# Optimization experiments

Hardware: AMD Instinct MI355X
Metric: run time of the kernel (lower is better)

The kernel has to match this reference:

```python
import jax, jax.numpy as jnp
import numpy as np

N = 50000
E = 800000
NODE_F = 128
HID = 96
TEMP_F = 10


def setup_inputs() -> dict:
    key = jax.random.key(0)
    ks = jax.random.split(key, 10)
    x = jax.random.normal(ks[0], (N, NODE_F), dtype=jnp.float32)
    edge_index = jax.random.randint(ks[1], (2, E), 0, N, dtype=jnp.int64)
    temporal = jax.random.normal(ks[2], (N, TEMP_F), dtype=jnp.float32)
    # GCNConv: lin weight [in, out] (no bias in lin), separate bias [out]
    W_gcn = jax.random.normal(ks[3], (NODE_F, HID), dtype=jnp.float32) / np.sqrt(NODE_F)
    b_gcn = jnp.zeros((HID,), dtype=jnp.float32)
    W1 = jax.random.normal(ks[4], (HID + TEMP_F, HID), dtype=jnp.float32) / np.sqrt(HID + TEMP_F)
    b1 = jax.random.normal(ks[5], (HID,), dtype=jnp.float32) * 0.01
    W2 = jax.random.normal(ks[6], (HID + NODE_F, 1), dtype=jnp.float32) / np.sqrt(HID + NODE_F)
    b2 = jax.random.normal(ks[7], (1,), dtype=jnp.float32) * 0.01
    return {"x": x, "edge_index": edge_index, "temporal": temporal,
            "W_gcn": W_gcn, "b_gcn": b_gcn, "W1": W1, "b1": b1, "W2": W2, "b2": b2}


def _gcn_conv(x, edge_index, W, b):
    n = x.shape[0]
    loop = jnp.arange(n, dtype=edge_index.dtype)
    src = jnp.concatenate([edge_index[0], loop])  # [E+N]
    dst = jnp.concatenate([edge_index[1], loop])
    # symmetric normalization with self-loops (PyG gcn_norm)
    ones = jnp.ones(src.shape[0], dtype=x.dtype)
    deg = jax.ops.segment_sum(ones, dst, num_segments=n)
    dinv = jnp.where(deg > 0, jax.lax.rsqrt(deg), 0.0)
    norm = dinv[src] * dinv[dst]  # [E+N]
    h = x @ W  # [N, HID]
    msg = h[src] * norm[:, None]  # [E+N, HID] gather + scale
    out = jax.ops.segment_sum(msg, dst, num_segments=n)  # scatter-add
    return out + b


def reference(x, edge_index, temporal, W_gcn, b_gcn, W1, b1, W2, b2):
    h = jax.nn.relu(_gcn_conv(x, edge_index, W_gcn, b_gcn))  # [N, HID]
    h = jnp.concatenate([h, temporal], axis=-1)              # [N, HID+TEMP_F]
    h = jax.nn.relu(h @ W1 + b1)                             # [N, HID]
    h = jnp.concatenate([h, x], axis=-1)                     # [N, HID+NODE_F]
    return jax.nn.relu(h @ W2 + b2)                          # [N, 1]
```

## Files before the change

### kernel.cpp

```cpp
#include <hip/hip_runtime.h>
#include <hip/hip_bf16.h>

#define NN 50000
#define NPAD 50048
#define NE 800000
#define NF 128
#define HH 96
#define TF 10
#define Z1DIM (HH + TF)
#define ZK 128
#define NCH 4
#define CW 24
#define CWP 32
#define NBK 196
#define CAP 5120
#define EPB 2048
#define FILLA_B ((NE + EPB - 1) / EPB)

#define WBLK (NF * HH / 4 / 256)
#define W1BLK (HH * ZK / 4 / 256)
#define ZPAD_JOBS 3
#define GEMM_JOBS (NPAD / 64)
#define AGG_JOBS (8 * 782)

typedef __attribute__((ext_vector_type(8))) short short8;
typedef __attribute__((ext_vector_type(8))) unsigned short ushort8;
typedef __attribute__((ext_vector_type(4))) float f32x4;

__device__ __forceinline__ float bu2f(unsigned short u) {
    union { unsigned int i; float f; } c;
    c.i = ((unsigned int)u) << 16;
    return c.f;
}
__device__ __forceinline__ unsigned short f2bu(float f) {
    union { __hip_bfloat16 h; unsigned short u; } c;
    c.h = __float2bfloat16(f);
    return c.u;
}
__device__ __forceinline__ float u2f32(unsigned short lo, unsigned short hi) {
    union { unsigned int i; float f; } c;
    c.i = ((unsigned int)hi << 16) | lo;
    return c.f;
}

__global__ void k_init(int* __restrict__ bcur, int* __restrict__ off) {
    int t = threadIdx.x;
    if (t < NBK) bcur[t] = t * CAP;
    if (t == 255) off[NN] = NE;
}

__global__ __launch_bounds__(256) void k_pre(const int* __restrict__ ei,
                                             int* __restrict__ bcur,
                                             int* __restrict__ temp,
                                             const float* __restrict__ W,
                                             const float* __restrict__ W1,
                                             unsigned short* __restrict__ Wt,
                                             unsigned short* __restrict__ Wt1,
                                             unsigned short* __restrict__ zb) {
    const int t = threadIdx.x;
    if (blockIdx.x < FILLA_B) {
        __shared__ int hist[NBK], bas[NBK];
        for (int m = t; m < NBK; m += 256) hist[m] = 0;
        __syncthreads();
        const int e0 = blockIdx.x * EPB;
        const int ecap = min(e0 + EPB, NE);
        for (int e = e0 + t; e < ecap; e += 256) {
            int d = ei[NE + e];
            atomicAdd(&hist[d >> 8], 1);
        }
        __syncthreads();
        for (int m = t; m < NBK; m += 256) {
            int c = hist[m];
            bas[m] = c ? atomicAdd(&bcur[m], c) : 0;
            hist[m] = 0;
        }
        __syncthreads();
        for (int e = e0 + t; e < ecap; e += 256) {
            int d = ei[NE + e], s = ei[e];
            int b = d >> 8;
            int r = atomicAdd(&hist[b], 1);
            temp[bas[b] + r] = ((d & 255) << 16) | s;
        }
        return;
    }
    int b = blockIdx.x - FILLA_B;
    if (b < WBLK) {
        int e = (b * 256 + t) * 4;
        int n = e >> 7, k = e & 127;
        ushort4 v;
        v.x = f2bu(W[(k + 0) * HH + n]);
        v.y = f2bu(W[(k + 1) * HH + n]);
        v.z = f2bu(W[(k + 2) * HH + n]);
        v.w = f2bu(W[(k + 3) * HH + n]);
        *(ushort4*)(Wt + e) = v;
    } else if (b < WBLK + W1BLK) {
        int e = ((b - WBLK) * 256 + t) * 4;
        int n = e >> 7, k = e & 127;
        ushort4 v;
        v.x = (k + 0 < Z1DIM) ? f2bu(W1[(k + 0) * HH + n]) : (unsigned short)0;
        v.y = (k + 1 < Z1DIM) ? f2bu(W1[(k + 1) * HH + n]) : (unsigned short)0;
        v.z = (k + 2 < Z1DIM) ? f2bu(W1[(k + 2) * HH + n]) : (unsigned short)0;
        v.w = (k + 3 < Z1DIM) ? f2bu(W1[(k + 3) * HH + n]) : (unsigned short)0;
        *(ushort4*)(Wt1 + e) = v;
    } else {
        int e8 = ((b - WBLK - W1BLK) * 256 + t) * 8;
        ushort8 z = {};
        *(ushort8*)(zb + (size_t)NN * ZK + e8) = z;
    }
}

__global__ __launch_bounds__(256) void k_gg(const int* __restrict__ temp,
                                            const int* __restrict__ bcur,
                                            unsigned short* __restrict__ csr,
                                            int* __restrict__ off,
                                            const float* __restrict__ x,
                                            const unsigned short* __restrict__ Wt,
                                            const float* __restrict__ W2,
                                            unsigned short* __restrict__ hp_c,
                                            float* __restrict__ xw2) {
    const int t = threadIdx.x;
    if (blockIdx.x < NBK) {
        __shared__ int ls[256], lc[256];
        const int b = blockIdx.x;
        int szt = (t < NBK) ? (bcur[t] - t * CAP) : 0;
        ls[t] = szt;
        __syncthreads();
#pragma unroll
        for (int d = 1; d < 256; d <<= 1) {
            int u = (t >= d) ? ls[t - d] : 0;
            __syncthreads();
            ls[t] += u;
            __syncthreads();
        }
        const int g0 = (b > 0) ? ls[b - 1] : 0;
        __syncthreads();
        ls[t] = 0;
        __syncthreads();
        const int seg0 = b * CAP;
        const int m = bcur[b] - seg0;
        for (int k = t; k < m; k += 256) atomicAdd(&ls[temp[seg0 + k] >> 16], 1);
        __syncthreads();
        const int myc = ls[t];
        lc[t] = myc;
        __syncthreads();
#pragma unroll
        for (int d = 1; d < 256; d <<= 1) {
            int u = (t >= d) ? lc[t - d] : 0;
            __syncthreads();
            lc[t] += u;
            __syncthreads();
        }
        const int myoff = g0 + lc[t] - myc;
        __syncthreads();
        lc[t] = myoff;
        const int i = b * 256 + t;
        if (i < NN) {
            off[i] = myoff;
            const float dinv = rsqrtf((float)myc + 1.f);
#pragma unroll
            for (int cc = 0; cc < NCH; ++cc)
                *(float*)(hp_c + (size_t)cc * NN * CWP + (size_t)i * CWP + 28) = dinv;
        } else if (i == NN) {
            off[NN] = NE;
        }
        __syncthreads();
        for (int k = t; k < m; k += 256) {
            int v = temp[seg0 + k];
            int r = atomicAdd(&lc[v >> 16], 1);
            csr[r] = (unsigned short)(v & 0xFFFF);
        }
        return;
    }
    const int wave = t >> 6;
    const int lane = t & 63;
    const int quad = lane >> 4;
    const int l16 = lane & 15;
    const int Mbase = (blockIdx.x - NBK) * 64 + wave * 16;
    const int row = Mbase + l16;
    const bool valid = row < NN;

    const float* xr = x + (size_t)row * NF + quad * 8;
    const unsigned short* brow = Wt + (size_t)l16 * NF + quad * 8;

    f32x4 acc[6] = {};
    float xs = 0.f;
#pragma unroll
    for (int ks = 0; ks < 4; ++ks) {
        short8 a = {};
        if (valid) {
            float4 f0 = *(const float4*)(xr + ks * 32);
            float4 f1 = *(const float4*)(xr + ks * 32 + 4);
            const float4 w0 = *(const float4*)(W2 + HH + quad * 8 + ks * 32);
            const float4 w1 = *(const float4*)(W2 + HH + quad * 8 + ks * 32 + 4);
            xs = fmaf(f0.x, w0.x, xs); xs = fmaf(f0.y, w0.y, xs);
            xs = fmaf(f0.z, w0.z, xs); xs = fmaf(f0.w, w0.w, xs);
            xs = fmaf(f1.x, w1.x, xs); xs = fmaf(f1.y, w1.y, xs);
            xs = fmaf(f1.z, w1.z, xs); xs = fmaf(f1.w, w1.w, xs);
            a[0] = (short)f2bu(f0.x); a[1] = (short)f2bu(f0.y);
            a[2] = (short)f2bu(f0.z); a[3] = (short)f2bu(f0.w);
            a[4] = (short)f2bu(f1.x); a[5] = (short)f2bu(f1.y);
            a[6] = (short)f2bu(f1.z); a[7] = (short)f2bu(f1.w);
        }
#pragma unroll
        for (int nt = 0; nt < 6; ++nt) {
            short8 bfrag = *(const short8*)(brow + (size_t)nt * 16 * NF + ks * 32);
            acc[nt] = __builtin_amdgcn_mfma_f32_16x16x32_bf16(a, bfrag, acc[nt], 0, 0, 0);
        }
    }
    xs += __shfl_xor(xs, 16, 64);
    xs += __shfl_xor(xs, 32, 64);
    if (quad == 0 && valid) xw2[row] = xs;

    const int r0 = Mbase + quad * 4;
#pragma unroll
    for (int nt = 0; nt < 6; ++nt) {
        int n = nt * 16 + l16;
        int c = n / CW, jj = n - c * CW;
        unsigned short* dst = hp_c + (size_t)c * NN * CWP + jj;
#pragma unroll
        for (int k = 0; k < 4; ++k)
            if (r0 + k < NN) dst[(size_t)(r0 + k) * CWP] = f2bu(acc[nt][k]);
    }
}

__global__ __launch_bounds__(256) void k_agg(const unsigned short* __restrict__ hp_c,
                                             const int* __restrict__ off,
                                             const unsigned short* __restrict__ csr,
                                             const float* __restrict__ bg,
                                             const float* __restrict__ tmp,
                                             unsigned short* __restrict__ zb) {
    const int b = blockIdx.x;
    const int slot = b & 7;
    const int c = slot >> 1;
    const int r = (b >> 3) * 2 + (slot & 1);
    const int item = r * 256 + threadIdx.x;
    if (item >= NN * 8) return;
    const int i = item >> 3;
    const int sub = item & 7;
    const int q = sub & 3;
    const int h = sub >> 2;
    const int lane = threadIdx.x & 63;
    const int srcl = lane | 3;
    const unsigned short* __restrict__ base = hp_c + (size_t)c * NN * CWP + q * 8;

    float a[8];
    if (h == 0) {
        ushort8 sv = *(const ushort8*)(base + (size_t)i * CWP);
        float dsl = __shfl(u2f32(sv[4], sv[5]), srcl, 64);
#pragma unroll
        for (int j = 0; j < 8; ++j) a[j] = dsl * bu2f(sv[j]);
    } else {
#pragma unroll
        for (int j = 0; j < 8; ++j) a[j] = 0.f;
    }

    const int start = off[i];
    const int end = off[i + 1];
    const int len = end - start;
    const float dv = rsqrtf((float)len + 1.f);
    const int half0 = (len + 1) >> 1;
    int k = h ? start + half0 : start;
    const int ke = h ? end : start + half0;
    for (; k + 3 < ke; k += 4) {
        int s0 = csr[k], s1 = csr[k + 1], s2 = csr[k + 2], s3 = csr[k + 3];
        ushort8 v0 = *(const ushort8*)(base + (size_t)s0 * CWP);
        ushort8 v1 = *(const ushort8*)(base + (size_t)s1 * CWP);
        ushort8 v2 = *(const ushort8*)(base + (size_t)s2 * CWP);
        ushort8 v3 = *(const ushort8*)(base + (size_t)s3 * CWP);
        float d0 = __shfl(u2f32(v0[4], v0[5]), srcl, 64);
        float d1 = __shfl(u2f32(v1[4], v1[5]), srcl, 64);
        float d2 = __shfl(u2f32(v2[4], v2[5]), srcl, 64);
        float d3 = __shfl(u2f32(v3[4], v3[5]), srcl, 64);
#pragma unroll
        for (int j = 0; j < 8; ++j) {
            float p0 = fmaf(d0, bu2f(v0[j]), a[j]);
            float p1 = fmaf(d2, bu2f(v2[j]), fmaf(d1, bu2f(v1[j]), 0.f));
            a[j] = fmaf(d3, bu2f(v3[j]), p0 + p1);
        }
    }
    for (; k < ke; ++k) {
        ushort8 v0 = *(const ushort8*)(base + (size_t)csr[k] * CWP);
        float d0 = __shfl(u2f32(v0[4], v0[5]), srcl, 64);
#pragma unroll
        for (int j = 0; j < 8; ++j) a[j] = fmaf(d0, bu2f(v0[j]), a[j]);
    }
#pragma unroll
    for (int j = 0; j < 8; ++j) a[j] += __shfl_xor(a[j], 4, 64);
    if (h == 0) {
        if (q < 3) {
            const int j0 = c * CW + q * 8;
            ushort8 o;
#pragma unroll
            for (int j = 0; j < 8; ++j)
                o[j] = f2bu(fmaxf(fmaf(dv, a[j], bg[j0 + j]), 0.f));
            *(ushort8*)(zb + (size_t)i * ZK + j0) = o;
        } else if (c == 3) {
            const float* tp = tmp + (size_t)i * TF;
            ushort8 o0, z = {};
#pragma unroll
            for (int j = 0; j < 8; ++j) o0[j] = f2bu(tp[j]);
            ushort8 o1 = z;
            o1[0] = f2bu(tp[8]);
            o1[1] = f2bu(tp[9]);
            unsigned short* zp = zb + (size_t)i * ZK + HH;
            *(ushort8*)(zp) = o0;
            *(ushort8*)(zp + 8) = o1;
            *(ushort8*)(zp + 16) = z;
            *(ushort8*)(zp + 24) = z;
        }
    }
}

__global__ __launch_bounds__(256) void k_mlp2(const unsigned short* __restrict__ zb,
                                              const unsigned short* __restrict__ Wt1,
                                              const float* __restrict__ b1,
                                              const float* __restrict__ W2,
                                              const float* __restrict__ b2,
                                              const float* __restrict__ xw2,
                                              float* __restrict__ out) {
    const int wave = threadIdx.x >> 6;
    const int lane = threadIdx.x & 63;
    const int quad = lane >> 4;
    const int l16 = lane & 15;
    const int Mbase = blockIdx.x * 64 + wave * 16;

    const unsigned short* arow = zb + (size_t)(Mbase + l16) * ZK + quad * 8;
    const unsigned short* brow = Wt1 + (size_t)l16 * ZK + quad * 8;

    f32x4 acc[6] = {};
#pragma unroll
    for (int ks = 0; ks < 4; ++ks) {
        short8 a = *(const short8*)(arow + ks * 32);
#pragma unroll
        for (int nt = 0; nt < 6; ++nt) {
            short8 bfrag = *(const short8*)(brow + (size_t)nt * 16 * ZK + ks * 32);
            acc[nt] = __builtin_amdgcn_mfma_f32_16x16x32_bf16(a, bfrag, acc[nt], 0, 0, 0);
        }
    }
    float bb[6], wa[6];
#pragma unroll
    for (int nt = 0; nt < 6; ++nt) {
        int c = nt * 16 + l16;
        bb[nt] = b1[c];
        wa[nt] = W2[c];
    }
    const float bias2 = b2[0];

#pragma unroll
    for (int reg = 0; reg < 4; ++reg) {
        const int r = Mbase + quad * 4 + reg;
        float p = 0.f;
#pragma unroll
        for (int nt = 0; nt < 6; ++nt)
            p = fmaf(fmaxf(acc[nt][reg] + bb[nt], 0.f), wa[nt], p);
#pragma unroll
        for (int m = 1; m < 16; m <<= 1) p += __shfl_xor(p, m, 64);
        if (l16 == 0 && r < NN) out[r] = fmaxf(p + xw2[r] + bias2, 0.f);
    }
}

extern "C" void kernel_launch(void* const* d_in, const int* in_sizes, int n_in,
                              void* d_out, int out_size, void* d_ws, size_t ws_size,
                              hipStream_t stream) {
    const float* x   = (const float*)d_in[0];
    const int*   ei  = (const int*)d_in[1];
    const float* tmp = (const float*)d_in[2];
    const float* Wg  = (const float*)d_in[3];
    const float* bg  = (const float*)d_in[4];
    const float* W1  = (const float*)d_in[5];
    const float* b1  = (const float*)d_in[6];
    const float* W2  = (const float*)d_in[7];
    const float* b2  = (const float*)d_in[8];
    float* out = (float*)d_out;

    char* base = (char*)d_ws;
    int* off  = (int*)base;
    int* bcur = (int*)(base + (256 << 10));
    unsigned short* csr = (unsigned short*)(base + (512 << 10));
    unsigned short* Wt  = (unsigned short*)(base + ((size_t)3 << 20));
    unsigned short* Wt1 = Wt + NF * HH;
    unsigned short* hp_c = (unsigned short*)(base + ((size_t)4 << 20));
    unsigned short* zb  = (unsigned short*)(base + ((size_t)17 << 20));
    float* xw2 = (float*)(base + ((size_t)30 << 20));
    int* temp  = (int*)(base + ((size_t)31 << 20));

    k_init <<<1, 256, 0, stream>>>(bcur, off);
    k_pre  <<<FILLA_B + WBLK + W1BLK + ZPAD_JOBS, 256, 0, stream>>>(
                ei, bcur, temp, Wg, W1, Wt, Wt1, zb);
    k_gg   <<<NBK + GEMM_JOBS, 256, 0, stream>>>(temp, bcur, csr, off, x, Wt, W2, hp_c, xw2);
    k_agg  <<<AGG_JOBS, 256, 0, stream>>>(hp_c, off, csr, bg, tmp, zb);
    k_mlp2 <<<GEMM_JOBS, 256, 0, stream>>>(zb, Wt1, b1, W2, b2, xw2, out);
}
```

Before: 169.2 us.

## Fuse GCN aggregation with MLP stage through shared-memory tile

```diff
diff --git a/kernel.cpp b/kernel.cpp
--- a/kernel.cpp
+++ b/kernel.cpp
@@ -19,9 +19,8 @@
 
 #define WBLK (NF * HH / 4 / 256)
 #define W1BLK (HH * ZK / 4 / 256)
-#define ZPAD_JOBS 3
 #define GEMM_JOBS (NPAD / 64)
-#define AGG_JOBS (8 * 782)
+#define ZTS 136
 
 typedef __attribute__((ext_vector_type(8))) short short8;
 typedef __attribute__((ext_vector_type(8))) unsigned short ushort8;
@@ -43,10 +42,9 @@
     return c.f;
 }
 
-__global__ void k_init(int* __restrict__ bcur, int* __restrict__ off) {
+__global__ void k_init(int* __restrict__ bcur) {
     int t = threadIdx.x;
     if (t < NBK) bcur[t] = t * CAP;
-    if (t == 255) off[NN] = NE;
 }
 
 __global__ __launch_bounds__(256) void k_pre(const int* __restrict__ ei,
@@ -55,8 +53,7 @@
                                              const float* __restrict__ W,
                                              const float* __restrict__ W1,
                                              unsigned short* __restrict__ Wt,
-                                             unsigned short* __restrict__ Wt1,
-                                             unsigned short* __restrict__ zb) {
+                                             unsigned short* __restrict__ Wt1) {
     const int t = threadIdx.x;
     if (blockIdx.x < FILLA_B) {
         __shared__ int hist[NBK], bas[NBK];
@@ -93,7 +90,7 @@
         v.z = f2bu(W[(k + 2) * HH + n]);
         v.w = f2bu(W[(k + 3) * HH + n]);
         *(ushort4*)(Wt + e) = v;
-    } else if (b < WBLK + W1BLK) {
+    } else {
         int e = ((b - WBLK) * 256 + t) * 4;
         int n = e >> 7, k = e & 127;
         ushort4 v;
@@ -102,10 +99,6 @@
         v.z = (k + 2 < Z1DIM) ? f2bu(W1[(k + 2) * HH + n]) : (unsigned short)0;
         v.w = (k + 3 < Z1DIM) ? f2bu(W1[(k + 3) * HH + n]) : (unsigned short)0;
         *(ushort4*)(Wt1 + e) = v;
-    } else {
-        int e8 = ((b - WBLK - W1BLK) * 256 + t) * 8;
-        ushort8 z = {};
-        *(ushort8*)(zb + (size_t)NN * ZK + e8) = z;
     }
 }
 
@@ -156,10 +149,7 @@
         const int i = b * 256 + t;
         if (i < NN) {
             off[i] = myoff;
-            const float dinv = rsqrtf((float)myc + 1.f);
-#pragma unroll
-            for (int cc = 0; cc < NCH; ++cc)
-                *(float*)(hp_c + (size_t)cc * NN * CWP + (size_t)i * CWP + 28) = dinv;
+            *(float*)(hp_c + (size_t)i * CWP + 28) = rsqrtf((float)myc + 1.f);
         } else if (i == NN) {
             off[NN] = NE;
         }
@@ -223,78 +213,95 @@
     }
 }
 
-__global__ __launch_bounds__(256) void k_agg(const unsigned short* __restrict__ hp_c,
-                                             const int* __restrict__ off,
-                                             const unsigned short* __restrict__ csr,
-                                             const float* __restrict__ bg,
-                                             const float* __restrict__ tmp,
-                                             unsigned short* __restrict__ zb) {
-    const int b = blockIdx.x;
-    const int slot = b & 7;
-    const int c = slot >> 1;
-    const int r = (b >> 3) * 2 + (slot & 1);
-    const int item = r * 256 + threadIdx.x;
-    if (item >= NN * 8) return;
-    const int i = item >> 3;
-    const int sub = item & 7;
-    const int q = sub & 3;
-    const int h = sub >> 2;
-    const int lane = threadIdx.x & 63;
+__global__ __launch_bounds__(256) void k_am(const unsigned short* __restrict__ hp_c,
+                                            const int* __restrict__ off,
+                                            const unsigned short* __restrict__ csr,
+                                            const float* __restrict__ bg,
+                                            const float* __restrict__ tmp,
+                                            const unsigned short* __restrict__ Wt1,
+                                            const float* __restrict__ b1,
+                                            const float* __restrict__ W2,
+                                            const float* __restrict__ b2,
+                                            const float* __restrict__ xw2,
+                                            float* __restrict__ out) {
+    __shared__ unsigned short zt[64][ZTS];
+    const int t = threadIdx.x;
+    const int n = t >> 2;
+    const int q = t & 3;
+    const int i = blockIdx.x * 64 + n;
+    const int lane = t & 63;
     const int srcl = lane | 3;
-    const unsigned short* __restrict__ base = hp_c + (size_t)c * NN * CWP + q * 8;
-
-    float a[8];
-    if (h == 0) {
-        ushort8 sv = *(const ushort8*)(base + (size_t)i * CWP);
-        float dsl = __shfl(u2f32(sv[4], sv[5]), srcl, 64);
-#pragma unroll
-        for (int j = 0; j < 8; ++j) a[j] = dsl * bu2f(sv[j]);
-    } else {
-#pragma unroll
-        for (int j = 0; j < 8; ++j) a[j] = 0.f;
-    }
-
-    const int start = off[i];
-    const int end = off[i + 1];
-    const int len = end - start;
-    const float dv = rsqrtf((float)len + 1.f);
-    const int half0 = (len + 1) >> 1;
-    int k = h ? start + half0 : start;
-    const int ke = h ? end : start + half0;
-    for (; k + 3 < ke; k += 4) {
-        int s0 = csr[k], s1 = csr[k + 1], s2 = csr[k + 2], s3 = csr[k + 3];
-        ushort8 v0 = *(const ushort8*)(base + (size_t)s0 * CWP);
-        ushort8 v1 = *(const ushort8*)(base + (size_t)s1 * CWP);
-        ushort8 v2 = *(const ushort8*)(base + (size_t)s2 * CWP);
-        ushort8 v3 = *(const ushort8*)(base + (size_t)s3 * CWP);
-        float d0 = __shfl(u2f32(v0[4], v0[5]), srcl, 64);
-        float d1 = __shfl(u2f32(v1[4], v1[5]), srcl, 64);
-        float d2 = __shfl(u2f32(v2[4], v2[5]), srcl, 64);
-        float d3 = __shfl(u2f32(v3[4], v3[5]), srcl, 64);
-#pragma unroll
-        for (int j = 0; j < 8; ++j) {
-            float p0 = fmaf(d0, bu2f(v0[j]), a[j]);
-            float p1 = fmaf(d2, bu2f(v2[j]), fmaf(d1, bu2f(v1[j]), 0.f));
-            a[j] = fmaf(d3, bu2f(v3[j]), p0 + p1);
-        }
-    }
-    for (; k < ke; ++k) {
-        ushort8 v0 = *(const ushort8*)(base + (size_t)csr[k] * CWP);
-        float d0 = __shfl(u2f32(v0[4], v0[5]), srcl, 64);
-#pragma unroll
-        for (int j = 0; j < 8; ++j) a[j] = fmaf(d0, bu2f(v0[j]), a[j]);
-    }
-#pragma unroll
-    for (int j = 0; j < 8; ++j) a[j] += __shfl_xor(a[j], 4, 64);
-    if (h == 0) {
+
+    if (i < NN) {
+        const unsigned short* __restrict__ b0 = hp_c + q * 8;
+        const unsigned short* __restrict__ b1c = hp_c + (size_t)1 * NN * CWP + q * 8;
+        const unsigned short* __restrict__ b2c = hp_c + (size_t)2 * NN * CWP + q * 8;
+        const unsigned short* __restrict__ b3c = hp_c + (size_t)3 * NN * CWP + q * 8;
+
+        float ac[4][8];
+        {
+            ushort8 s0 = *(const ushort8*)(b0 + (size_t)i * CWP);
+            ushort8 s1 = *(const ushort8*)(b1c + (size_t)i * CWP);
+            ushort8 s2 = *(const ushort8*)(b2c + (size_t)i * CWP);
+            ushort8 s3 = *(const ushort8*)(b3c + (size_t)i * CWP);
+            float dsl = __shfl(u2f32(s0[4], s0[5]), srcl, 64);
+#pragma unroll
+            for (int j = 0; j < 8; ++j) {
+                ac[0][j] = dsl * bu2f(s0[j]);
+                ac[1][j] = dsl * bu2f(s1[j]);
+                ac[2][j] = dsl * bu2f(s2[j]);
+                ac[3][j] = dsl * bu2f(s3[j]);
+            }
+        }
+        int k = off[i];
+        const int ke = off[i + 1];
+        const float dv = rsqrtf((float)(ke - k) + 1.f);
+        for (; k + 1 < ke; k += 2) {
+            int sA = csr[k], sB = csr[k + 1];
+            ushort8 vA0 = *(const ushort8*)(b0 + (size_t)sA * CWP);
+            ushort8 vA1 = *(const ushort8*)(b1c + (size_t)sA * CWP);
+            ushort8 vA2 = *(const ushort8*)(b2c + (size_t)sA * CWP);
+            ushort8 vA3 = *(const ushort8*)(b3c + (size_t)sA * CWP);
+            ushort8 vB0 = *(const ushort8*)(b0 + (size_t)sB * CWP);
+            ushort8 vB1 = *(const ushort8*)(b1c + (size_t)sB * CWP);
+            ushort8 vB2 = *(const ushort8*)(b2c + (size_t)sB * CWP);
+            ushort8 vB3 = *(const ushort8*)(b3c + (size_t)sB * CWP);
+            float dA = __shfl(u2f32(vA0[4], vA0[5]), srcl, 64);
+            float dB = __shfl(u2f32(vB0[4], vB0[5]), srcl, 64);
+#pragma unroll
+            for (int j = 0; j < 8; ++j) {
+                ac[0][j] = fmaf(dB, bu2f(vB0[j]), fmaf(dA, bu2f(vA0[j]), ac[0][j]));
+                ac[1][j] = fmaf(dB, bu2f(vB1[j]), fmaf(dA, bu2f(vA1[j]), ac[1][j]));
+                ac[2][j] = fmaf(dB, bu2f(vB2[j]), fmaf(dA, bu2f(vA2[j]), ac[2][j]));
+                ac[3][j] = fmaf(dB, bu2f(vB3[j]), fmaf(dA, bu2f(vA3[j]), ac[3][j]));
+            }
+        }
+        if (k < ke) {
+            int sA = csr[k];
+            ushort8 vA0 = *(const ushort8*)(b0 + (size_t)sA * CWP);
+            ushort8 vA1 = *(const ushort8*)(b1c + (size_t)sA * CWP);
+            ushort8 vA2 = *(const ushort8*)(b2c + (size_t)sA * CWP);
+            ushort8 vA3 = *(const ushort8*)(b3c + (size_t)sA * CWP);
+            float dA = __shfl(u2f32(vA0[4], vA0[5]), srcl, 64);
+#pragma unroll
+            for (int j = 0; j < 8; ++j) {
+                ac[0][j] = fmaf(dA, bu2f(vA0[j]), ac[0][j]);
+                ac[1][j] = fmaf(dA, bu2f(vA1[j]), ac[1][j]);
+                ac[2][j] = fmaf(dA, bu2f(vA2[j]), ac[2][j]);
+                ac[3][j] = fmaf(dA, bu2f(vA3[j]), ac[3][j]);
+            }
+        }
         if (q < 3) {
-            const int j0 = c * CW + q * 8;
-            ushort8 o;
-#pragma unroll
-            for (int j = 0; j < 8; ++j)
-                o[j] = f2bu(fmaxf(fmaf(dv, a[j], bg[j0 + j]), 0.f));
-            *(ushort8*)(zb + (size_t)i * ZK + j0) = o;
-        } else if (c == 3) {
+#pragma unroll
+            for (int c = 0; c < 4; ++c) {
+                const int j0 = c * CW + q * 8;
+                ushort8 o;
+#pragma unroll
+                for (int j = 0; j < 8; ++j)
+                    o[j] = f2bu(fmaxf(fmaf(dv, ac[c][j], bg[j0 + j]), 0.f));
+                *(ushort8*)(&zt[n][j0]) = o;
+            }
+        } else {
             const float* tp = tmp + (size_t)i * TF;
             ushort8 o0, z = {};
 #pragma unroll
@@ -302,35 +309,42 @@
             ushort8 o1 = z;
             o1[0] = f2bu(tp[8]);
             o1[1] = f2bu(tp[9]);
-            unsigned short* zp = zb + (size_t)i * ZK + HH;
-            *(ushort8*)(zp) = o0;
-            *(ushort8*)(zp + 8) = o1;
-            *(ushort8*)(zp + 16) = z;
-            *(ushort8*)(zp + 24) = z;
-        }
-    }
-}
-
-__global__ __launch_bounds__(256) void k_mlp2(const unsigned short* __restrict__ zb,
-                                              const unsigned short* __restrict__ Wt1,
-                                              const float* __restrict__ b1,
-                                              const float* __restrict__ W2,
-                                              const float* __restrict__ b2,
-                                              const float* __restrict__ xw2,
-                                              float* __restrict__ out) {
-    const int wave = threadIdx.x >> 6;
-    const int lane = threadIdx.x & 63;
-    const int quad = lane >> 4;
+            *(ushort8*)(&zt[n][96]) = o0;
+            *(ushort8*)(&zt[n][104]) = o1;
+            *(ushort8*)(&zt[n][112]) = z;
+            *(ushort8*)(&zt[n][120]) = z;
+            *(ushort8*)(&zt[n][128]) = z;
+        }
+    } else {
+        if (q < 3) {
+#pragma unroll
+            for (int c = 0; c < 4; ++c) {
+                ushort8 z = {};
+                *(ushort8*)(&zt[n][c * CW + q * 8]) = z;
+            }
+        } else {
+            ushort8 z = {};
+            *(ushort8*)(&zt[n][96]) = z;
+            *(ushort8*)(&zt[n][104]) = z;
+            *(ushort8*)(&zt[n][112]) = z;
+            *(ushort8*)(&zt[n][120]) = z;
+            *(ushort8*)(&zt[n][128]) = z;
+        }
+    }
+    __syncthreads();
+
+    const int wave = t >> 6;
+    const int quadB = lane >> 4;
     const int l16 = lane & 15;
+    const int Mrow = wave * 16 + l16;
     const int Mbase = blockIdx.x * 64 + wave * 16;
 
-    const unsigned short* arow = zb + (size_t)(Mbase + l16) * ZK + quad * 8;
-    const unsigned short* brow = Wt1 + (size_t)l16 * ZK + quad * 8;
+    const unsigned short* brow = Wt1 + (size_t)l16 * ZK + quadB * 8;
 
     f32x4 acc[6] = {};
 #pragma unroll
     for (int ks = 0; ks < 4; ++ks) {
-        short8 a = *(const short8*)(arow + ks * 32);
+        short8 a = *(const short8*)(&zt[Mrow][quadB * 8 + ks * 32]);
 #pragma unroll
         for (int nt = 0; nt < 6; ++nt) {
             short8 bfrag = *(const short8*)(brow + (size_t)nt * 16 * ZK + ks * 32);
@@ -340,15 +354,15 @@
     float bb[6], wa[6];
 #pragma unroll
     for (int nt = 0; nt < 6; ++nt) {
-        int c = nt * 16 + l16;
-        bb[nt] = b1[c];
-        wa[nt] = W2[c];
+        int cc = nt * 16 + l16;
+        bb[nt] = b1[cc];
+        wa[nt] = W2[cc];
     }
     const float bias2 = b2[0];
 
 #pragma unroll
     for (int reg = 0; reg < 4; ++reg) {
-        const int r = Mbase + quad * 4 + reg;
+        const int r = Mbase + quadB * 4 + reg;
         float p = 0.f;
 #pragma unroll
         for (int nt = 0; nt < 6; ++nt)
@@ -380,14 +394,11 @@
     unsigned short* Wt  = (unsigned short*)(base + ((size_t)3 << 20));
     unsigned short* Wt1 = Wt + NF * HH;
     unsigned short* hp_c = (unsigned short*)(base + ((size_t)4 << 20));
-    unsigned short* zb  = (unsigned short*)(base + ((size_t)17 << 20));
-    float* xw2 = (float*)(base + ((size_t)30 << 20));
-    int* temp  = (int*)(base + ((size_t)31 << 20));
-
-    k_init <<<1, 256, 0, stream>>>(bcur, off);
-    k_pre  <<<FILLA_B + WBLK + W1BLK + ZPAD_JOBS, 256, 0, stream>>>(
-                ei, bcur, temp, Wg, W1, Wt, Wt1, zb);
+    float* xw2 = (float*)(base + ((size_t)17 << 20));
+    int* temp  = (int*)(base + ((size_t)18 << 20));
+
+    k_init <<<1, 256, 0, stream>>>(bcur);
+    k_pre  <<<FILLA_B + WBLK + W1BLK, 256, 0, stream>>>(ei, bcur, temp, Wg, W1, Wt, Wt1);
     k_gg   <<<NBK + GEMM_JOBS, 256, 0, stream>>>(temp, bcur, csr, off, x, Wt, W2, hp_c, xw2);
-    k_agg  <<<AGG_JOBS, 256, 0, stream>>>(hp_c, off, csr, bg, tmp, zb);
-    k_mlp2 <<<GEMM_JOBS, 256, 0, stream>>>(zb, Wt1, b1, W2, b2, xw2, out);
-}
+    k_am   <<<GEMM_JOBS, 256, 0, stream>>>(hp_c, off, csr, bg, tmp, Wt1, b1, W2, b2, xw2, out);
+}
```

Measured after the change: 188.2 us. 11.2% more time.
